# Optimization experiments

Hardware: AMD Instinct MI355X
Metric: run time of the kernel (lower is better)

The kernel has to match this reference:

```python
import jax, jax.numpy as jnp
from jax import lax
import numpy as np

B, IMG, P, CIN, D, DEPTH, H, FF = 32, 512, 16, 4, 256, 4, 8, 2048
N = (IMG // P) ** 2          # 1024 patches
L = N // 2                   # exactly 512 masked patches per batch (static max_len)
DH = D // H
EPS = 1e-5


def layer_norm(x, s, b):
    m = x.mean(-1, keepdims=True)
    v = ((x - m) ** 2).mean(-1, keepdims=True)
    return (x - m) * lax.rsqrt(v + EPS) * s + b


def setup_inputs() -> dict:
    key = jax.random.key(0)
    ks = jax.random.split(key, 16)
    init = lambda k, shp: 0.02 * jax.random.normal(k, shp, jnp.float32)

    image = jax.random.normal(ks[0], (B, 3, IMG, IMG), jnp.float32)
    # patch-granular binary mask: exactly L patches per batch have value 0 (masked)
    scores = jax.random.uniform(ks[1], (B, N))
    idx = jnp.argsort(scores, axis=1)[:, :L]
    pm = jnp.ones((B, N), jnp.float32).at[jnp.arange(B)[:, None], idx].set(0.0)
    mask = jnp.repeat(jnp.repeat(pm.reshape(B, 1, IMG // P, IMG // P), P, 2), P, 3)

    return dict(
        image=image, mask=mask,
        conv_w=init(ks[2], (D, CIN, P, P)), conv_b=jnp.zeros((D,), jnp.float32),
        pos_embed=jax.random.normal(ks[3], (1, N, D), jnp.float32),
        qkv_w=init(ks[4], (DEPTH, D, 3 * D)), qkv_b=jnp.zeros((DEPTH, 3 * D), jnp.float32),
        out_w=init(ks[5], (DEPTH, D, D)), out_b=jnp.zeros((DEPTH, D), jnp.float32),
        ln1_s=jnp.ones((DEPTH, D), jnp.float32), ln1_b=jnp.zeros((DEPTH, D), jnp.float32),
        ff1_w=init(ks[6], (DEPTH, D, FF)), ff1_b=jnp.zeros((DEPTH, FF), jnp.float32),
        ff2_w=init(ks[7], (DEPTH, FF, D)), ff2_b=jnp.zeros((DEPTH, D), jnp.float32),
        ln2_s=jnp.ones((DEPTH, D), jnp.float32), ln2_b=jnp.zeros((DEPTH, D), jnp.float32),
    )


def reference(image, mask, conv_w, conv_b, pos_embed, qkv_w, qkv_b, out_w, out_b,
              ln1_s, ln1_b, ff1_w, ff1_b, ff2_w, ff2_b, ln2_s, ln2_b):
    xin = jnp.concatenate([image, mask], axis=1)                       # [B,4,512,512]
    x = lax.conv_general_dilated(xin, conv_w, (P, P), 'VALID',
                                 dimension_numbers=('NCHW', 'OIHW', 'NCHW'))
    x = x + conv_b[None, :, None, None]                                # [B,D,32,32]
    Bc = x.shape[0]
    x = x.reshape(Bc, D, N).transpose(0, 2, 1)                         # [B,N,D]

    # nearest downsample (factor exactly P): sample at indices i*P
    pmask = mask[:, 0, ::P, ::P].reshape(Bc, N)
    sel = pmask < 0.5                                                  # masked patches
    # stable compaction: indices of masked patches first, in original order
    order = jnp.argsort(jnp.logical_not(sel), axis=1, stable=True)[:, :L]
    tokens = jnp.take_along_axis(x, order[..., None], axis=1)          # [B,L,D]
    pos = pos_embed[0][order]                                          # [B,L,D]
    lengths = sel.sum(axis=1)
    valid = (jnp.arange(L)[None, :] < lengths[:, None])[..., None]
    h = jnp.where(valid, tokens + pos, 0.0)                            # zero padding

    scale = 1.0 / np.sqrt(DH)
    for i in range(DEPTH):  # post-norm torch TransformerEncoderLayer, no dropout
        qkv = h @ qkv_w[i] + qkv_b[i]
        q, k, v = jnp.split(qkv, 3, axis=-1)
        q = q.reshape(Bc, L, H, DH)
        k = k.reshape(Bc, L, H, DH)
        v = v.reshape(Bc, L, H, DH)
        att = jax.nn.softmax(jnp.einsum('bqhd,bkhd->bhqk', q, k) * scale, axis=-1)
        o = jnp.einsum('bhqk,bkhd->bqhd', att, v).reshape(Bc, L, D)
        h = layer_norm(h + o @ out_w[i] + out_b[i], ln1_s[i], ln1_b[i])
        ff = jax.nn.relu(h @ ff1_w[i] + ff1_b[i]) @ ff2_w[i] + ff2_b[i]
        h = layer_norm(h + ff, ln2_s[i], ln2_b[i])
    return h
```

## Files before the change

kernel.cpp:

```cpp
#include <hip/hip_runtime.h>
#include <cstdint>
#include <cstddef>


#define Bq 32
#define Dm 256
#define Lq 512
#define Hh 8
#define FFq 2048
#define Mtok (Bq * Lq)

typedef __attribute__((ext_vector_type(8))) short  short8;
typedef __attribute__((ext_vector_type(4))) float  f32x4;
typedef __attribute__((ext_vector_type(4))) unsigned int u32x4;
typedef __attribute__((ext_vector_type(2))) unsigned int u32x2;

static __device__ __forceinline__ unsigned short f2bf(float f) {
    unsigned int u = __float_as_uint(f);
    unsigned int r = (u + 0x7FFFu + ((u >> 16) & 1u)) >> 16;
    return (unsigned short)r;
}
static __device__ __forceinline__ unsigned int pk2bf(float lo, float hi) {
    return (unsigned int)f2bf(lo) | ((unsigned int)f2bf(hi) << 16);
}

static __device__ __forceinline__ void gload_lds16(const void* g, void* l) {
    __builtin_amdgcn_global_load_lds(
        (const __attribute__((address_space(1))) unsigned int*)g,
        (__attribute__((address_space(3))) unsigned int*)l, 16, 0, 0);
}

__global__ __launch_bounds__(1024) void k_order(const float* __restrict__ mask,
                                                int* __restrict__ order) {
    const int b = blockIdx.x;
    const int n = threadIdx.x;
    const float v = mask[(size_t)b * 262144 + (size_t)(n >> 5) * 8192 + (n & 31) * 16];
    const bool sel = v < 0.5f;
    const unsigned long long ball = __ballot(sel);
    const int wave = n >> 6, lane = n & 63;
    __shared__ int wsum[16];
    __shared__ int wpre[16];
    if (lane == 0) wsum[wave] = __popcll(ball);
    __syncthreads();
    if (n == 0) {
        int s = 0;
        for (int i = 0; i < 16; ++i) { wpre[i] = s; s += wsum[i]; }
    }
    __syncthreads();
    const int rank = wpre[wave] + __popcll(ball & ((1ull << lane) - 1ull));
    if (sel) order[b * Lq + rank] = n;
}

__global__ __launch_bounds__(256) void k_gather(const float* __restrict__ image,
                                                const int* __restrict__ order,
                                                const float* __restrict__ pos,
                                                unsigned short* __restrict__ patchA,
                                                float* __restrict__ posG) {
    __shared__ int pn[16];
    const int tid = threadIdx.x;
    const int tok0 = blockIdx.x * 16;
    if (tid < 16) pn[tid] = order[tok0 + tid];
    __syncthreads();
    const int lane = tid & 63, w4 = tid >> 6;
    const int rr = lane >> 2, col4 = (lane & 3) << 2;
#pragma unroll
    for (int it = 0; it < 12; ++it) {
        const int s = it * 4 + w4;
        const int t = s / 3, cch = s % 3;
        const int n = pn[t];
        const int b = (tok0 + t) >> 9;
        const int pi = n >> 5, pj = n & 31;
        const float4 v = *(const float4*)&image[
            (((size_t)b * 3 + cch) * 512 + pi * 16 + rr) * 512 + pj * 16 + col4];
        unsigned int pk[2] = {pk2bf(v.x, v.y), pk2bf(v.z, v.w)};
        *(uint2*)&patchA[(size_t)(tok0 + t) * 768 + cch * 256 + rr * 16 + col4] =
            *(uint2*)pk;
    }
#pragma unroll
    for (int it = 0; it < 4; ++it) {
        const int t = it * 4 + w4;
        *(float4*)&posG[(size_t)(tok0 + t) * Dm + lane * 4] =
            *(const float4*)&pos[(size_t)pn[t] * Dm + lane * 4];
    }
}

__global__ __launch_bounds__(256) void k_wembed(const float* __restrict__ conv_w,
                                                unsigned short* __restrict__ W16) {
    const int i = blockIdx.x * 256 + threadIdx.x;
    const int d = i / 96, k8 = (i % 96) * 8;
    const float4 a = *(const float4*)&conv_w[(size_t)d * 1024 + k8];
    const float4 b = *(const float4*)&conv_w[(size_t)d * 1024 + k8 + 4];
    unsigned int pk[4] = {pk2bf(a.x, a.y), pk2bf(a.z, a.w),
                          pk2bf(b.x, b.y), pk2bf(b.z, b.w)};
    *(uint4*)&W16[(size_t)d * 768 + k8] = *(uint4*)pk;
}

__global__ __launch_bounds__(256) void k_wprep_all(const float* __restrict__ qkv_w,
                                                   const float* __restrict__ out_w,
                                                   const float* __restrict__ ff1_w,
                                                   const float* __restrict__ ff2_w,
                                                   unsigned short* __restrict__ Wq,
                                                   unsigned short* __restrict__ Wo,
                                                   unsigned short* __restrict__ Wf1,
                                                   unsigned short* __restrict__ Wf2) {
    __shared__ float tile[64][65];
    int idx = blockIdx.x;
    const float* W; unsigned short* WT; int K, N, l, r;
    if (idx < 192)      { l = idx / 48;          r = idx % 48;  K = 256;  N = 768;  W = qkv_w; WT = Wq; }
    else if (idx < 256) { l = (idx - 192) / 16;  r = idx & 15;  K = 256;  N = 256;  W = out_w; WT = Wo; }
    else if (idx < 768) { l = (idx - 256) / 128; r = (idx - 256) % 128; K = 256;  N = 2048; W = ff1_w; WT = Wf1; }
    else                { l = (idx - 768) / 128; r = (idx - 768) % 128; K = 2048; N = 256;  W = ff2_w; WT = Wf2; }
    const int nTiles = N >> 6;
    const int n0 = (r % nTiles) * 64, k0 = (r / nTiles) * 64;
    W  += (size_t)l * K * N;
    WT += (size_t)l * K * N;
    const int t = threadIdx.x;
#pragma unroll
    for (int it = 0; it < 4; ++it) {
        const int rr = (t >> 4) + it * 16, c4 = (t & 15) * 4;
        *(float4*)&tile[rr][c4] = *(const float4*)&W[(size_t)(k0 + rr) * N + n0 + c4];
    }
    __syncthreads();
    const int n = t & 63, kq = t >> 6;
    unsigned short pk[16];
#pragma unroll
    for (int j = 0; j < 16; ++j) pk[j] = f2bf(tile[kq * 16 + j][n]);
    unsigned short* dst = &WT[(size_t)(n0 + n) * K + k0 + kq * 16];
    *(uint4*)dst       = *(uint4*)&pk[0];
    *(uint4*)(dst + 8) = *(uint4*)&pk[8];
}

template <bool RELU, bool RES, bool OUT32, bool OUT16, int NBUF>
__global__ __launch_bounds__(256) void k_mgemm(const unsigned short* __restrict__ A,
                                               const unsigned short* __restrict__ W,
                                               const float* __restrict__ bias,
                                               const float* __restrict__ R,
                                               float* __restrict__ C32,
                                               unsigned short* __restrict__ C16,
                                               int M, int N, int K) {
    __shared__ unsigned short Al[128 * 64 * NBUF];
    __shared__ unsigned short Bl[128 * 64 * NBUF];
    const int tid = threadIdx.x;
    const int lane = tid & 63, wave = tid >> 6;
    const int wm = wave >> 1, wn = wave & 1;
    const int m0 = blockIdx.y * 128, n0 = blockIdx.x * 128;
    const int c = lane >> 4, a15 = lane & 15;
    f32x4 acc[4][4] = {};

    const int srow = lane >> 3;
    const int sgran = (lane & 7) ^ srow;
    const int KT = K >> 6;

    auto stage = [&](int buf, int kt) {
        const int k0 = kt << 6;
#pragma unroll
        for (int q = 0; q < 4; ++q) {
            const int rbase = wave * 32 + q * 8;
            gload_lds16(A + (size_t)(m0 + rbase + srow) * K + k0 + sgran * 8,
                        &Al[buf * 8192 + rbase * 64]);
            gload_lds16(W + (size_t)(n0 + rbase + srow) * K + k0 + sgran * 8,
                        &Bl[buf * 8192 + rbase * 64]);
        }
    };
    auto compute = [&](int buf) {
        const int bo = buf * 8192;
#pragma unroll
        for (int kc = 0; kc < 2; ++kc) {
            short8 af[4], bf[4];
#pragma unroll
            for (int fm = 0; fm < 4; ++fm) {
                const int row = wm * 64 + fm * 16 + a15;
                const int slot = (kc * 4 + c) ^ (row & 7);
                af[fm] = *(const short8*)&Al[bo + row * 64 + slot * 8];
            }
#pragma unroll
            for (int fn = 0; fn < 4; ++fn) {
                const int row = wn * 64 + fn * 16 + a15;
                const int slot = (kc * 4 + c) ^ (row & 7);
                bf[fn] = *(const short8*)&Bl[bo + row * 64 + slot * 8];
            }
#pragma unroll
            for (int fm = 0; fm < 4; ++fm)
#pragma unroll
                for (int fn = 0; fn < 4; ++fn)
                    acc[fm][fn] = __builtin_amdgcn_mfma_f32_16x16x32_bf16(
                        af[fm], bf[fn], acc[fm][fn], 0, 0, 0);
        }
    };

    if constexpr (NBUF == 2) {
        stage(0, 0);
        for (int kt = 0; kt < KT; ++kt) {
            const int cur = kt & 1;
            if (kt + 1 < KT) {
                stage(cur ^ 1, kt + 1);
                asm volatile("s_waitcnt vmcnt(8)" ::: "memory");
            } else {
                asm volatile("s_waitcnt vmcnt(0)" ::: "memory");
            }
            __builtin_amdgcn_s_barrier();
            compute(cur);
            __builtin_amdgcn_s_barrier();
        }
    } else {
        for (int kt = 0; kt < KT; ++kt) {
            __syncthreads();
            stage(0, kt);
            __syncthreads();
            compute(0);
        }
    }
#pragma unroll
    for (int fn = 0; fn < 4; ++fn) {
        const int col = n0 + wn * 64 + fn * 16 + a15;
        const float bv = bias[col];
#pragma unroll
        for (int fm = 0; fm < 4; ++fm) {
            const int mrow = m0 + wm * 64 + fm * 16 + c * 4;
#pragma unroll
            for (int r = 0; r < 4; ++r) {
                float v = acc[fm][fn][r] + bv;
                if constexpr (RES) v += R[(size_t)(mrow + r) * N + col];
                if constexpr (RELU) v = fmaxf(v, 0.f);
                if constexpr (OUT32) C32[(size_t)(mrow + r) * N + col] = v;
                if constexpr (OUT16) C16[(size_t)(mrow + r) * N + col] = f2bf(v);
            }
        }
    }
}

__global__ __launch_bounds__(256) void k_gemm_ln(const unsigned short* __restrict__ A,
                                                 const unsigned short* __restrict__ W,
                                                 const float* __restrict__ bias,
                                                 const float* __restrict__ R,
                                                 const float* __restrict__ lns,
                                                 const float* __restrict__ lnb,
                                                 float* __restrict__ Y32,
                                                 unsigned short* __restrict__ Y16,
                                                 int K) {
    __shared__ unsigned short Al[32 * 64 * 2];
    __shared__ unsigned short Bl[256 * 64 * 2];
    __shared__ float redS[4][32];
    __shared__ float redQ[4][32];
    const int tid = threadIdx.x;
    const int lane = tid & 63, wave = tid >> 6;
    const int m0 = blockIdx.x * 32;
    const int c = lane >> 4, a15 = lane & 15;
    f32x4 acc[2][4] = {};

    const int srow = lane >> 3;
    const int sgran = (lane & 7) ^ srow;
    const int KT = K >> 6;

    auto stage = [&](int buf, int kt) {
        const int k0 = kt << 6;
        gload_lds16(A + (size_t)(m0 + wave * 8 + srow) * K + k0 + sgran * 8,
                    &Al[buf * 2048 + (wave * 8) * 64]);
#pragma unroll
        for (int q = 0; q < 8; ++q) {
            const int rbase = wave * 64 + q * 8;
            gload_lds16(W + (size_t)(rbase + srow) * K + k0 + sgran * 8,
                        &Bl[buf * 16384 + rbase * 64]);
        }
    };
    auto compute = [&](int buf) {
        const int ao = buf * 2048, bo = buf * 16384;
#pragma unroll
        for (int kc = 0; kc < 2; ++kc) {
            short8 af[2], bf[4];
#pragma unroll
            for (int fm = 0; fm < 2; ++fm) {
                const int row = fm * 16 + a15;
                const int slot = (kc * 4 + c) ^ (row & 7);
                af[fm] = *(const short8*)&Al[ao + row * 64 + slot * 8];
            }
#pragma unroll
            for (int fn = 0; fn < 4; ++fn) {
                const int row = wave * 64 + fn * 16 + a15;
                const int slot = (kc * 4 + c) ^ (row & 7);
                bf[fn] = *(const short8*)&Bl[bo + row * 64 + slot * 8];
            }
#pragma unroll
            for (int fm = 0; fm < 2; ++fm)
#pragma unroll
                for (int fn = 0; fn < 4; ++fn)
                    acc[fm][fn] = __builtin_amdgcn_mfma_f32_16x16x32_bf16(
                        af[fm], bf[fn], acc[fm][fn], 0, 0, 0);
        }
    };

    stage(0, 0);
    for (int kt = 0; kt < KT; ++kt) {
        const int cur = kt & 1;
        if (kt + 1 < KT) {
            stage(cur ^ 1, kt + 1);
            asm volatile("s_waitcnt vmcnt(9)" ::: "memory");
        } else {
            asm volatile("s_waitcnt vmcnt(0)" ::: "memory");
        }
        __builtin_amdgcn_s_barrier();
        compute(cur);
        __builtin_amdgcn_s_barrier();
    }

    float bv[4], sg[4], bg[4];
#pragma unroll
    for (int fn = 0; fn < 4; ++fn) {
        const int col = wave * 64 + fn * 16 + a15;
        bv[fn] = bias[col]; sg[fn] = lns[col]; bg[fn] = lnb[col];
    }
#pragma unroll
    for (int fm = 0; fm < 2; ++fm) {
        const int mrow = m0 + fm * 16 + c * 4;
#pragma unroll
        for (int r = 0; r < 4; ++r) {
            float ps = 0.f, pq = 0.f;
#pragma unroll
            for (int fn = 0; fn < 4; ++fn) {
                const int col = wave * 64 + fn * 16 + a15;
                float v = acc[fm][fn][r] + bv[fn] + R[(size_t)(mrow + r) * Dm + col];
                acc[fm][fn][r] = v;
                ps += v; pq += v * v;
            }
#pragma unroll
            for (int off = 1; off < 16; off <<= 1) {
                ps += __shfl_xor(ps, off);
                pq += __shfl_xor(pq, off);
            }
            if (a15 == 0) {
                redS[wave][fm * 16 + c * 4 + r] = ps;
                redQ[wave][fm * 16 + c * 4 + r] = pq;
            }
        }
    }
    __syncthreads();
#pragma unroll
    for (int fm = 0; fm < 2; ++fm) {
        const int lrow = fm * 16 + c * 4;
        const int mrow = m0 + lrow;
#pragma unroll
        for (int r = 0; r < 4; ++r) {
            const float totS = redS[0][lrow + r] + redS[1][lrow + r] +
                               redS[2][lrow + r] + redS[3][lrow + r];
            const float totQ = redQ[0][lrow + r] + redQ[1][lrow + r] +
                               redQ[2][lrow + r] + redQ[3][lrow + r];
            const float mean = totS * (1.f / 256.f);
            const float var = totQ * (1.f / 256.f) - mean * mean;
            const float inv = rsqrtf(var + 1e-5f);
#pragma unroll
            for (int fn = 0; fn < 4; ++fn) {
                const int col = wave * 64 + fn * 16 + a15;
                const float y = (acc[fm][fn][r] - mean) * inv * sg[fn] + bg[fn];
                Y32[(size_t)(mrow + r) * Dm + col] = y;
                Y16[(size_t)(mrow + r) * Dm + col] = f2bf(y);
            }
        }
    }
}

__global__ __launch_bounds__(512) void k_attn(const unsigned short* __restrict__ QKV,
                                              unsigned short* __restrict__ O) {
    __shared__ unsigned short Kl[512 * 32];
    __shared__ unsigned short Vt[32 * 512];
    const int bh = blockIdx.x, b = bh >> 3, h = bh & 7;
    const int tid = threadIdx.x, lane = tid & 63, wave = tid >> 6;
    const int c = lane >> 4, a15 = lane & 15;
    const size_t qkvbase = (size_t)b * Lq * 768 + h * 32;

    {
        const int srow = lane >> 2;
        const int sg = (lane & 3) ^ ((srow >> 1) & 3);
#pragma unroll
        for (int q = 0; q < 4; ++q) {
            const int rbase = wave * 64 + q * 16;
            gload_lds16(QKV + qkvbase + (size_t)(rbase + srow) * 768 + 256 + sg * 8,
                        &Kl[rbase * 32]);
        }
    }
    {
        const int kg = tid & 127, dg = tid >> 7;
        u32x4 v[4];
#pragma unroll
        for (int kk = 0; kk < 4; ++kk)
            v[kk] = *(const u32x4*)&QKV[qkvbase + (size_t)(kg * 4 + kk) * 768 + 512 + dg * 8];
#pragma unroll
        for (int dd = 0; dd < 8; ++dd) {
            const int d = dg * 8 + dd;
            unsigned short e[4];
#pragma unroll
            for (int kk = 0; kk < 4; ++kk) {
                const unsigned int word = v[kk][dd >> 1];
                e[kk] = (dd & 1) ? (unsigned short)(word >> 16) : (unsigned short)(word & 0xffff);
            }
            unsigned int pk[2];
            pk[0] = (unsigned int)e[0] | ((unsigned int)e[1] << 16);
            pk[1] = (unsigned int)e[2] | ((unsigned int)e[3] << 16);
            *(uint2*)&Vt[d * 512 + ((kg ^ (d & 7)) << 2)] = *(uint2*)pk;
        }
    }
    const int q0w = wave * 64;
    short8 qf[4];
#pragma unroll
    for (int fn = 0; fn < 4; ++fn)
        qf[fn] = *(const short8*)&QKV[qkvbase + (size_t)(q0w + fn * 16 + a15) * 768 + c * 8];
    __syncthreads();

    const float scale = 0.17677669529663687f;
    f32x4 oacc[2][4] = {};
    float mstat[4], lstat[4];
#pragma unroll
    for (int fn = 0; fn < 4; ++fn) { mstat[fn] = -1e30f; lstat[fn] = 0.f; }
    const f32x4 zero4 = {0.f, 0.f, 0.f, 0.f};

    for (int t = 0; t < 16; ++t) {
        const int kv0 = t * 32;
        short8 kf[2];
#pragma unroll
        for (int fm = 0; fm < 2; ++fm) {
            const int row = kv0 + fm * 16 + a15;
            const int slot = c ^ ((row >> 1) & 3);
            kf[fm] = *(const short8*)&Kl[row * 32 + slot * 8];
        }
        short8 vf[2];
#pragma unroll
        for (int fmd = 0; fmd < 2; ++fmd) {
            const int d = fmd * 16 + a15;
            const int g0 = (t * 8 + c) ^ (d & 7);
            const int g1 = (t * 8 + 4 + c) ^ (d & 7);
            const u32x2 r0 = *(const u32x2*)&Vt[d * 512 + g0 * 4];
            const u32x2 r1 = *(const u32x2*)&Vt[d * 512 + g1 * 4];
            const u32x4 cmb = {r0[0], r0[1], r1[0], r1[1]};
            vf[fmd] = __builtin_bit_cast(short8, cmb);
        }
        f32x4 s[2][4];
#pragma unroll
        for (int fm = 0; fm < 2; ++fm)
#pragma unroll
            for (int fn = 0; fn < 4; ++fn)
                s[fm][fn] = __builtin_amdgcn_mfma_f32_16x16x32_bf16(kf[fm], qf[fn], zero4, 0, 0, 0);
#pragma unroll
        for (int fn = 0; fn < 4; ++fn) {
            float p[8];
            float tmax = -1e30f;
#pragma unroll
            for (int fm = 0; fm < 2; ++fm)
#pragma unroll
                for (int r = 0; r < 4; ++r) {
                    const float x = s[fm][fn][r] * scale;
                    p[fm * 4 + r] = x;
                    tmax = fmaxf(tmax, x);
                }
            tmax = fmaxf(tmax, __shfl_xor(tmax, 16));
            tmax = fmaxf(tmax, __shfl_xor(tmax, 32));
            const float mnew = fmaxf(mstat[fn], tmax);
            const float alpha = __expf(mstat[fn] - mnew);
            mstat[fn] = mnew;
            float tsum = 0.f;
            short8 pf;
#pragma unroll
            for (int j = 0; j < 8; ++j) {
                const float e = __expf(p[j] - mnew);
                tsum += e;
                pf[j] = (short)f2bf(e);
            }
            tsum += __shfl_xor(tsum, 16);
            tsum += __shfl_xor(tsum, 32);
            lstat[fn] = lstat[fn] * alpha + tsum;
#pragma unroll
            for (int fmd = 0; fmd < 2; ++fmd) {
                oacc[fmd][fn] *= alpha;
                oacc[fmd][fn] = __builtin_amdgcn_mfma_f32_16x16x32_bf16(
                    vf[fmd], pf, oacc[fmd][fn], 0, 0, 0);
            }
        }
    }
#pragma unroll
    for (int fn = 0; fn < 4; ++fn) {
        const float invl = 1.f / lstat[fn];
        const size_t qrow = (size_t)(b * Lq + q0w + fn * 16 + a15);
#pragma unroll
        for (int fmd = 0; fmd < 2; ++fmd)
#pragma unroll
            for (int r = 0; r < 4; ++r)
                O[qrow * Dm + h * 32 + fmd * 16 + c * 4 + r] = f2bf(oacc[fmd][fn][r] * invl);
    }
}

extern "C" void kernel_launch(void* const* d_in, const int* in_sizes, int n_in,
                              void* d_out, int out_size, void* d_ws, size_t ws_size,
                              hipStream_t stream) {
    const float* image  = (const float*)d_in[0];
    const float* mask   = (const float*)d_in[1];
    const float* conv_w = (const float*)d_in[2];
    const float* conv_b = (const float*)d_in[3];
    const float* pos    = (const float*)d_in[4];
    const float* qkv_w  = (const float*)d_in[5];
    const float* qkv_b  = (const float*)d_in[6];
    const float* out_w  = (const float*)d_in[7];
    const float* out_b  = (const float*)d_in[8];
    const float* ln1_s  = (const float*)d_in[9];
    const float* ln1_b  = (const float*)d_in[10];
    const float* ff1_w  = (const float*)d_in[11];
    const float* ff1_b  = (const float*)d_in[12];
    const float* ff2_w  = (const float*)d_in[13];
    const float* ff2_b  = (const float*)d_in[14];
    const float* ln2_s  = (const float*)d_in[15];
    const float* ln2_b  = (const float*)d_in[16];
    float* out = (float*)d_out;

    char* w = (char*)d_ws;
    int* order            = (int*)w;            w += 64 * 1024;
    float* H32            = (float*)w;          w += (size_t)Mtok * Dm * 4;
    unsigned short* H16   = (unsigned short*)w; w += (size_t)Mtok * Dm * 2;
    unsigned short* QKV16 = (unsigned short*)w; w += (size_t)Mtok * 768 * 2;
    unsigned short* O16   = (unsigned short*)w; w += (size_t)Mtok * Dm * 2;
    unsigned short* F16   = (unsigned short*)w; w += (size_t)Mtok * FFq * 2;
    unsigned short* Wq    = (unsigned short*)w; w += (size_t)4 * 768 * 256 * 2;
    unsigned short* Wo    = (unsigned short*)w; w += (size_t)4 * 256 * 256 * 2;
    unsigned short* Wf1   = (unsigned short*)w; w += (size_t)4 * 2048 * 256 * 2;
    unsigned short* Wf2   = (unsigned short*)w; w += (size_t)4 * 256 * 2048 * 2;
    unsigned short* We    = (unsigned short*)w; w += (size_t)256 * 768 * 2;
    unsigned short* patchA = F16;
    float* posG            = (float*)(F16 + (size_t)Mtok * 768);

    k_order<<<Bq, 1024, 0, stream>>>(mask, order);
    k_gather<<<Mtok / 16, 256, 0, stream>>>(image, order, pos, patchA, posG);
    k_wembed<<<96, 256, 0, stream>>>(conv_w, We);
    k_wprep_all<<<1280, 256, 0, stream>>>(qkv_w, out_w, ff1_w, ff2_w, Wq, Wo, Wf1, Wf2);

    k_mgemm<false, true, true, true, 2><<<dim3(2, 128), 256, 0, stream>>>(
        patchA, We, conv_b, posG, H32, H16, Mtok, 256, 768);

    for (int i = 0; i < 4; ++i) {
        k_mgemm<false, false, false, true, 1><<<dim3(6, 128), 256, 0, stream>>>(
            H16, Wq + (size_t)i * 768 * 256, qkv_b + (size_t)i * 768, nullptr,
            nullptr, QKV16, Mtok, 768, 256);
        k_attn<<<Bq * Hh, 512, 0, stream>>>(QKV16, O16);
        k_gemm_ln<<<Mtok / 32, 256, 0, stream>>>(
            O16, Wo + (size_t)i * 256 * 256, out_b + (size_t)i * 256, H32,
            ln1_s + i * Dm, ln1_b + i * Dm, H32, H16, 256);
        k_mgemm<true, false, false, true, 1><<<dim3(16, 128), 256, 0, stream>>>(
            H16, Wf1 + (size_t)i * 2048 * 256, ff1_b + (size_t)i * FFq, nullptr,
            nullptr, F16, Mtok, 2048, 256);
        float* dst32 = (i == 3) ? out : H32;
        k_gemm_ln<<<Mtok / 32, 256, 0, stream>>>(
            F16, Wf2 + (size_t)i * 256 * 2048, ff2_b + (size_t)i * 256, H32,
            ln2_s + i * Dm, ln2_b + i * Dm, dst32, H16, 2048);
    }
    (void)in_sizes; (void)n_in; (void)out_size; (void)ws_size;
}
```

Baseline: 605.8 us.

## Fuse FFN up-projection, ReLU, down-projection and layernorm into one kernel

```diff
diff --git a/kernel.cpp b/kernel.cpp
--- a/kernel.cpp
+++ b/kernel.cpp
@@ -351,6 +351,146 @@
             for (int fn = 0; fn < 4; ++fn) {
                 const int col = wave * 64 + fn * 16 + a15;
                 const float y = (acc[fm][fn][r] - mean) * inv * sg[fn] + bg[fn];
+                Y32[(size_t)(mrow + r) * Dm + col] = y;
+                Y16[(size_t)(mrow + r) * Dm + col] = f2bf(y);
+            }
+        }
+    }
+}
+
+__global__ __launch_bounds__(256) void k_ff_ln(const unsigned short* __restrict__ A,
+                                               const unsigned short* __restrict__ W1,
+                                               const unsigned short* __restrict__ W2,
+                                               const float* __restrict__ b1,
+                                               const float* __restrict__ b2,
+                                               const float* __restrict__ R,
+                                               const float* __restrict__ lns,
+                                               const float* __restrict__ lnb,
+                                               float* __restrict__ Y32,
+                                               unsigned short* __restrict__ Y16) {
+    __shared__ unsigned short A32[32 * 256];
+    __shared__ unsigned short W1s[32 * 256];
+    __shared__ unsigned short W2s[256 * 32];
+    __shared__ unsigned short Pl[32 * 40];
+    __shared__ float redS[4][32];
+    __shared__ float redQ[4][32];
+    const int tid = threadIdx.x;
+    const int lane = tid & 63, wave = tid >> 6;
+    const int m0 = blockIdx.x * 32;
+    const int c = lane >> 4, a15 = lane & 15;
+    const int mf = wave & 1, nf = wave >> 1;
+
+    const int srow2 = lane >> 5, g32 = lane & 31;
+    const int srow16 = lane >> 2, g4 = lane & 3;
+
+#pragma unroll
+    for (int q = 0; q < 4; ++q) {
+        const int rbase = (wave * 4 + q) * 2;
+        const int row = rbase + srow2;
+        gload_lds16(A + (size_t)(m0 + row) * 256 + (g32 ^ (row & 7)) * 8,
+                    &A32[rbase * 256]);
+    }
+
+    f32x4 acc2[2][4] = {};
+
+    for (int fc = 0; fc < 64; ++fc) {
+        __builtin_amdgcn_s_barrier();
+#pragma unroll
+        for (int q = 0; q < 4; ++q) {
+            const int rbase = (wave * 4 + q) * 2;
+            const int row = rbase + srow2;
+            gload_lds16(W1 + (size_t)(fc * 32 + row) * 256 + (g32 ^ (row & 7)) * 8,
+                        &W1s[rbase * 256]);
+        }
+#pragma unroll
+        for (int q = 0; q < 4; ++q) {
+            const int rbase = (wave * 4 + q) * 16;
+            const int row = rbase + srow16;
+            gload_lds16(W2 + (size_t)row * 2048 + fc * 32 + (g4 ^ ((row >> 1) & 3)) * 8,
+                        &W2s[rbase * 32]);
+        }
+        asm volatile("s_waitcnt vmcnt(0)" ::: "memory");
+        __builtin_amdgcn_s_barrier();
+        f32x4 acc1 = {0.f, 0.f, 0.f, 0.f};
+#pragma unroll
+        for (int ks = 0; ks < 8; ++ks) {
+            const int arow = mf * 16 + a15;
+            const short8 af = *(const short8*)&A32[arow * 256 + (((ks * 4 + c) ^ (arow & 7)) * 8)];
+            const int wrow = nf * 16 + a15;
+            const short8 wf = *(const short8*)&W1s[wrow * 256 + (((ks * 4 + c) ^ (wrow & 7)) * 8)];
+            acc1 = __builtin_amdgcn_mfma_f32_16x16x32_bf16(af, wf, acc1, 0, 0, 0);
+        }
+        const float bb1 = b1[fc * 32 + nf * 16 + a15];
+        const int pc = nf * 16 + a15;
+#pragma unroll
+        for (int r = 0; r < 4; ++r) {
+            const int pr = mf * 16 + c * 4 + r;
+            Pl[pr * 40 + pc] = f2bf(fmaxf(acc1[r] + bb1, 0.f));
+        }
+        __syncthreads();
+        short8 pa[2];
+#pragma unroll
+        for (int fm = 0; fm < 2; ++fm)
+            pa[fm] = *(const short8*)&Pl[(fm * 16 + a15) * 40 + c * 8];
+#pragma unroll
+        for (int fn = 0; fn < 4; ++fn) {
+            const int wrow = wave * 64 + fn * 16 + a15;
+            const short8 wb = *(const short8*)&W2s[wrow * 32 + ((c ^ ((wrow >> 1) & 3)) * 8)];
+#pragma unroll
+            for (int fm = 0; fm < 2; ++fm)
+                acc2[fm][fn] = __builtin_amdgcn_mfma_f32_16x16x32_bf16(
+                    pa[fm], wb, acc2[fm][fn], 0, 0, 0);
+        }
+    }
+
+    float bv[4], sg[4], bg[4];
+#pragma unroll
+    for (int fn = 0; fn < 4; ++fn) {
+        const int col = wave * 64 + fn * 16 + a15;
+        bv[fn] = b2[col]; sg[fn] = lns[col]; bg[fn] = lnb[col];
+    }
+#pragma unroll
+    for (int fm = 0; fm < 2; ++fm) {
+        const int mrow = m0 + fm * 16 + c * 4;
+#pragma unroll
+        for (int r = 0; r < 4; ++r) {
+            float ps = 0.f, pq = 0.f;
+#pragma unroll
+            for (int fn = 0; fn < 4; ++fn) {
+                const int col = wave * 64 + fn * 16 + a15;
+                float v = acc2[fm][fn][r] + bv[fn] + R[(size_t)(mrow + r) * Dm + col];
+                acc2[fm][fn][r] = v;
+                ps += v; pq += v * v;
+            }
+#pragma unroll
+            for (int off = 1; off < 16; off <<= 1) {
+                ps += __shfl_xor(ps, off);
+                pq += __shfl_xor(pq, off);
+            }
+            if (a15 == 0) {
+                redS[wave][fm * 16 + c * 4 + r] = ps;
+                redQ[wave][fm * 16 + c * 4 + r] = pq;
+            }
+        }
+    }
+    __syncthreads();
+#pragma unroll
+    for (int fm = 0; fm < 2; ++fm) {
+        const int lrow = fm * 16 + c * 4;
+        const int mrow = m0 + lrow;
+#pragma unroll
+        for (int r = 0; r < 4; ++r) {
+            const float totS = redS[0][lrow + r] + redS[1][lrow + r] +
+                               redS[2][lrow + r] + redS[3][lrow + r];
+            const float totQ = redQ[0][lrow + r] + redQ[1][lrow + r] +
+                               redQ[2][lrow + r] + redQ[3][lrow + r];
+            const float mean = totS * (1.f / 256.f);
+            const float var = totQ * (1.f / 256.f) - mean * mean;
+            const float inv = rsqrtf(var + 1e-5f);
+#pragma unroll
+            for (int fn = 0; fn < 4; ++fn) {
+                const int col = wave * 64 + fn * 16 + a15;
+                const float y = (acc2[fm][fn][r] - mean) * inv * sg[fn] + bg[fn];
                 Y32[(size_t)(mrow + r) * Dm + col] = y;
                 Y16[(size_t)(mrow + r) * Dm + col] = f2bf(y);
             }
@@ -509,19 +649,18 @@
     float* out = (float*)d_out;
 
     char* w = (char*)d_ws;
-    int* order            = (int*)w;            w += 64 * 1024;
-    float* H32            = (float*)w;          w += (size_t)Mtok * Dm * 4;
-    unsigned short* H16   = (unsigned short*)w; w += (size_t)Mtok * Dm * 2;
-    unsigned short* QKV16 = (unsigned short*)w; w += (size_t)Mtok * 768 * 2;
-    unsigned short* O16   = (unsigned short*)w; w += (size_t)Mtok * Dm * 2;
-    unsigned short* F16   = (unsigned short*)w; w += (size_t)Mtok * FFq * 2;
-    unsigned short* Wq    = (unsigned short*)w; w += (size_t)4 * 768 * 256 * 2;
-    unsigned short* Wo    = (unsigned short*)w; w += (size_t)4 * 256 * 256 * 2;
-    unsigned short* Wf1   = (unsigned short*)w; w += (size_t)4 * 2048 * 256 * 2;
-    unsigned short* Wf2   = (unsigned short*)w; w += (size_t)4 * 256 * 2048 * 2;
-    unsigned short* We    = (unsigned short*)w; w += (size_t)256 * 768 * 2;
-    unsigned short* patchA = F16;
-    float* posG            = (float*)(F16 + (size_t)Mtok * 768);
+    int* order             = (int*)w;            w += 64 * 1024;
+    float* H32             = (float*)w;          w += (size_t)Mtok * Dm * 4;
+    unsigned short* H16    = (unsigned short*)w; w += (size_t)Mtok * Dm * 2;
+    unsigned short* QKV16  = (unsigned short*)w; w += (size_t)Mtok * 768 * 2;
+    unsigned short* O16    = (unsigned short*)w; w += (size_t)Mtok * Dm * 2;
+    unsigned short* patchA = (unsigned short*)w; w += (size_t)Mtok * 768 * 2;
+    float* posG            = (float*)w;          w += (size_t)Mtok * Dm * 4;
+    unsigned short* Wq     = (unsigned short*)w; w += (size_t)4 * 768 * 256 * 2;
+    unsigned short* Wo     = (unsigned short*)w; w += (size_t)4 * 256 * 256 * 2;
+    unsigned short* Wf1    = (unsigned short*)w; w += (size_t)4 * 2048 * 256 * 2;
+    unsigned short* Wf2    = (unsigned short*)w; w += (size_t)4 * 256 * 2048 * 2;
+    unsigned short* We     = (unsigned short*)w; w += (size_t)256 * 768 * 2;
 
     k_order<<<Bq, 1024, 0, stream>>>(mask, order);
     k_gather<<<Mtok / 16, 256, 0, stream>>>(image, order, pos, patchA, posG);
@@ -539,13 +678,11 @@
         k_gemm_ln<<<Mtok / 32, 256, 0, stream>>>(
             O16, Wo + (size_t)i * 256 * 256, out_b + (size_t)i * 256, H32,
             ln1_s + i * Dm, ln1_b + i * Dm, H32, H16, 256);
-        k_mgemm<true, false, false, true, 1><<<dim3(16, 128), 256, 0, stream>>>(
-            H16, Wf1 + (size_t)i * 2048 * 256, ff1_b + (size_t)i * FFq, nullptr,
-            nullptr, F16, Mtok, 2048, 256);
         float* dst32 = (i == 3) ? out : H32;
-        k_gemm_ln<<<Mtok / 32, 256, 0, stream>>>(
-            F16, Wf2 + (size_t)i * 256 * 2048, ff2_b + (size_t)i * 256, H32,
-            ln2_s + i * Dm, ln2_b + i * Dm, dst32, H16, 2048);
+        k_ff_ln<<<Mtok / 32, 256, 0, stream>>>(
+            H16, Wf1 + (size_t)i * 2048 * 256, Wf2 + (size_t)i * 256 * 2048,
+            ff1_b + (size_t)i * FFq, ff2_b + (size_t)i * 256, H32,
+            ln2_s + i * Dm, ln2_b + i * Dm, dst32, H16);
     }
     (void)in_sizes; (void)n_in; (void)out_size; (void)ws_size;
 }
```

After: 823.3 us. 1.36x slower.
